# Kernel tuning notes

Hardware: AMD Instinct MI355X
Metric: run time of the kernel (lower is better)

The kernel has to match this reference:

```python
import jax, jax.numpy as jnp
import numpy as np

N = 16384      # total nodes (B graphs x 64 squares)
B = 256        # number of graphs
NODES = 64     # nodes per graph (chess board)
E = 131072     # directed edges (avg degree 8)
F_IN = 128
H = 256
GH = 4         # GAT heads
TH = 8         # transformer heads
L_GNN = 8
L_TF = 6
EPS = 1e-5


def layer_norm(x, g, b):
    m = jnp.mean(x, -1, keepdims=True)
    v = jnp.mean((x - m) ** 2, -1, keepdims=True)
    return (x - m) * jax.lax.rsqrt(v + EPS) * g + b


def setup_inputs() -> dict:
    key = jax.random.key(0)
    ks = iter(jax.random.split(key, 80))

    def nrm(shape, s=0.02):
        return jax.random.normal(next(ks), shape, jnp.float32) * s

    x = jax.random.normal(next(ks), (N, F_IN), jnp.float32)
    gid = jax.random.randint(next(ks), (E,), 0, B)
    off = jax.random.randint(next(ks), (2, E), 0, NODES)
    edge_index = gid[None, :] * NODES + off          # edges stay within a graph
    batch = jnp.arange(N, dtype=jnp.int32) // NODES
    piece_types = jax.random.randint(next(ks), (N,), 1, 7)
    return dict(
        x=x, edge_index=edge_index, batch=batch, piece_types=piece_types,
        emb_w=nrm((H, F_IN)), emb_b=nrm((H,)),
        gat_w=nrm((L_GNN, GH * H, H)), gat_as=nrm((L_GNN, GH, H)),
        gat_ad=nrm((L_GNN, GH, H)), gat_b=nrm((L_GNN, H)),
        gnn_g=jnp.ones((L_GNN, H)), gnn_beta=jnp.zeros((L_GNN, H)),
        ln1_g=jnp.ones((L_TF, H)), ln1_b=jnp.zeros((L_TF, H)),
        in_w=nrm((L_TF, 3 * H, H)), in_b=nrm((L_TF, 3 * H)),
        out_w=nrm((L_TF, H, H)), out_b=nrm((L_TF, H)),
        ln2_g=jnp.ones((L_TF, H)), ln2_b=jnp.zeros((L_TF, H)),
        ff1_w=nrm((L_TF, 4 * H, H)), ff1_b=nrm((L_TF, 4 * H)),
        ff2_w=nrm((L_TF, H, 4 * H)), ff2_b=nrm((L_TF, H)),
        pool_w=nrm((H,)), pool_b=nrm((1,)),
        vw1=nrm((H, H)), vb1=nrm((H,)), vw2=nrm((1, H)), vb2=nrm((1,)),
        pw1=nrm((H, H)), pb1=nrm((H,)), pw2=nrm((H, H)), pb2=nrm((H,)),
        uw1=nrm((H // 2, H)), ub1=nrm((H // 2,)), uw2=nrm((1, H // 2)), ub2=nrm((1,)))


def _forward(x, edge_index, batch, emb_w, emb_b, gat_w, gat_as, gat_ad, gat_b,
             gnn_g, gnn_beta, ln1_g, ln1_b, in_w, in_b, out_w, out_b, ln2_g,
             ln2_b, ff1_w, ff1_b, ff2_w, ff2_b, pool_w, pool_b, vw1, vb1, vw2,
             vb2, pw1, pb1, pw2, pb2, uw1, ub1, uw2, ub2):
    loops = jnp.arange(N, dtype=edge_index.dtype)     # GATConv add_self_loops=True
    src = jnp.concatenate([edge_index[0], loops])
    dst = jnp.concatenate([edge_index[1], loops])
    h = x @ emb_w.T + emb_b                           # [N,H] node embedding

    def gnn_layer(h, p):                              # ResidualGNNLayer
        W, a_s, a_d, bias, g, beta = p
        hp = (h @ W.T).reshape(N, GH, H)              # per-head projection
        al_s = jnp.sum(hp * a_s, -1)                  # [N,GH]
        al_d = jnp.sum(hp * a_d, -1)
        e = jax.nn.leaky_relu(al_s[src] + al_d[dst], 0.2)
        m = jax.ops.segment_max(e, dst, num_segments=N)
        ex = jnp.exp(e - m[dst])                      # segment softmax over dst
        den = jax.ops.segment_sum(ex, dst, num_segments=N)
        alpha = ex / den[dst]
        out = jax.ops.segment_sum(hp[src] * alpha[:, :, None], dst, num_segments=N)
        out = out.mean(1) + bias                      # concat=False -> head mean
        out = jax.nn.gelu(layer_norm(out, g, beta), approximate=False)
        return h + out, None                          # project = Identity

    h, _ = jax.lax.scan(gnn_layer, h, (gat_w, gat_as, gat_ad, gat_b, gnn_g, gnn_beta))

    # nn.MultiheadAttention defaults batch_first=False: axis0 (=B graphs) is the
    # sequence axis, axis1 (=64 nodes) is the batch axis — faithful to the source.
    xt = h.reshape(B, NODES, H)
    HD = H // TH

    def tf_layer(t, p):
        g1, b1, iw, ib, ow, ob, g2, b2, w1, fb1, w2, fb2 = p
        tn = layer_norm(t, g1, b1)
        q, k, v = jnp.split(tn @ iw.T + ib, 3, axis=-1)
        q = q.reshape(B, NODES, TH, HD)
        k = k.reshape(B, NODES, TH, HD)
        v = v.reshape(B, NODES, TH, HD)
        att = jnp.einsum('sbhd,tbhd->bhst', q, k) * (1.0 / HD ** 0.5)
        att = jax.nn.softmax(att, -1)
        o = jnp.einsum('bhst,tbhd->sbhd', att, v).reshape(B, NODES, H)
        t = t + (o @ ow.T + ob)
        tn = layer_norm(t, g2, b2)
        ff = jax.nn.gelu(tn @ w1.T + fb1, approximate=False) @ w2.T + fb2
        return t + ff, None

    xt, _ = jax.lax.scan(tf_layer, xt, (ln1_g, ln1_b, in_w, in_b, out_w, out_b,
                                        ln2_g, ln2_b, ff1_w, ff1_b, ff2_w, ff2_b))
    h = xt.reshape(N, H)

    # global attention pooling: softmax over ALL nodes (dim=0, as in the source)
    aw = jax.nn.softmax(h @ pool_w + pool_b[0], axis=0)
    g_rep = jax.ops.segment_sum(h * aw[:, None], batch, num_segments=B)
    value = jnp.tanh(jax.nn.gelu(g_rep @ vw1.T + vb1, approximate=False) @ vw2.T + vb2)[:, 0]
    policy = jax.nn.gelu(h @ pw1.T + pb1, approximate=False) @ pw2.T + pb2
    unc = jax.nn.softplus(jax.nn.gelu(g_rep @ uw1.T + ub1, approximate=False) @ uw2.T + ub2)[:, 0]
    return value, policy, unc


def reference(x, edge_index, batch, piece_types, emb_w, emb_b, gat_w, gat_as,
              gat_ad, gat_b, gnn_g, gnn_beta, ln1_g, ln1_b, in_w, in_b, out_w,
              out_b, ln2_g, ln2_b, ff1_w, ff1_b, ff2_w, ff2_b, pool_w, pool_b,
              vw1, vb1, vw2, vb2, pw1, pb1, pw2, pb2, uw1, ub1, uw2, ub2):
    # piece_types feeds PositionSpecificFeatureExtractor whose output is dead
    # code in the source forward (never used), so it is omitted here.
    return _forward(x, edge_index, batch, emb_w, emb_b, gat_w, gat_as, gat_ad,
                    gat_b, gnn_g, gnn_beta, ln1_g, ln1_b, in_w, in_b, out_w,
                    out_b, ln2_g, ln2_b, ff1_w, ff1_b, ff2_w, ff2_b, pool_w,
                    pool_b, vw1, vb1, vw2, vb2, pw1, pb1, pw2, pb2, uw1, ub1,
                    uw2, ub2)
```

## Files before the change

### kernel.cpp

```cpp
#include <hip/hip_runtime.h>
#include <hip/hip_bf16.h>

typedef __hip_bfloat16 bf16;
typedef __bf16 bf16x8 __attribute__((ext_vector_type(8)));
typedef float  f32x4  __attribute__((ext_vector_type(4)));

#define N_NODES 16384
#define HDIM    256
#define NE      131072
#define NE2     147456

__device__ __forceinline__ float b2f(bf16 v){ return __bfloat162float(v); }
__device__ __forceinline__ bf16  f2b(float v){ return __float2bfloat16(v); }
__device__ __forceinline__ float us2f(unsigned short u){
  union { unsigned int i; float f; } c; c.i = ((unsigned int)u) << 16; return c.f;
}
__device__ __forceinline__ unsigned short f2us(float f){
  bf16 h = __float2bfloat16(f);
  unsigned short u; __builtin_memcpy(&u, &h, 2); return u;
}
__device__ __forceinline__ float gelu_f(float x){
  return 0.5f * x * (1.0f + erff(x * 0.7071067811865476f));
}
__device__ __forceinline__ float wave_sum(float v){
  #pragma unroll
  for (int o = 32; o > 0; o >>= 1) v += __shfl_xor(v, o);
  return v;
}
__device__ __forceinline__ float wave_max(float v){
  #pragma unroll
  for (int o = 32; o > 0; o >>= 1) v = fmaxf(v, __shfl_xor(v, o));
  return v;
}

__device__ __forceinline__ float4 load4(const float* p){ return *(const float4*)p; }
__device__ __forceinline__ float4 load4(const bf16* p){
  ushort4 u = *(const ushort4*)p;
  return make_float4(us2f(u.x), us2f(u.y), us2f(u.z), us2f(u.w));
}
__device__ __forceinline__ void store4(float* p, float4 v){ *(float4*)p = v; }
__device__ __forceinline__ void store4(bf16* p, float4 v){
  ushort4 u = make_ushort4(f2us(v.x), f2us(v.y), f2us(v.z), f2us(v.w));
  *(ushort4*)p = u;
}
__device__ __forceinline__ void storev(float* p, float4 v){ *(float4*)p = v; }
__device__ __forceinline__ void storev(bf16*  p, float4 v){ store4(p, v); }

__device__ __forceinline__ void async_ld16(const bf16* g, unsigned short* l){
  __builtin_amdgcn_global_load_lds(
      (const __attribute__((address_space(1))) void*)g,
      (__attribute__((address_space(3))) void*)l, 16, 0, 0);
}

__global__ void detect_dtype(const unsigned short* __restrict__ x, int n, int* __restrict__ flags){
  int i = blockIdx.x * 256 + threadIdx.x;
  if (i < n) {
    unsigned short u = x[i];
    if ((u & 0x7F80) == 0x7F80) atomicOr(&flags[1], 1);
  }
}
struct ConvArgs {
  const void* src[35];
  unsigned short* dst[35];
  int cumg[36];
  int n[35];
};
__global__ void conv_all4(ConvArgs a, const int* __restrict__ flags){
  int gi = blockIdx.x * 256 + threadIdx.x;
  if (gi >= a.cumg[35]) return;
  int lo = 0, hi = 34;
  while (lo < hi) { int mid = (lo + hi + 1) >> 1; if (gi >= a.cumg[mid]) lo = mid; else hi = mid - 1; }
  int e0 = (gi - a.cumg[lo]) << 2;
  int n = a.n[lo];
  unsigned short* d = a.dst[lo];
  if (flags[1]) {
    const float* s = (const float*)a.src[lo];
    if (e0 + 4 <= n) {
      float4 v = *(const float4*)(s + e0);
      *(ushort4*)(d + e0) = make_ushort4(f2us(v.x), f2us(v.y), f2us(v.z), f2us(v.w));
    } else {
      for (int t = 0; t < n - e0; ++t) d[e0 + t] = f2us(s[e0 + t]);
    }
  } else {
    const unsigned short* s = (const unsigned short*)a.src[lo];
    if (e0 + 4 <= n) *(ushort4*)(d + e0) = *(const ushort4*)(s + e0);
    else for (int t = 0; t < n - e0; ++t) d[e0 + t] = s[e0 + t];
  }
}
__global__ void emit_out(const unsigned short* __restrict__ stage, void* __restrict__ out,
                         int n, const int* __restrict__ flags){
  int i = blockIdx.x * 256 + threadIdx.x;
  if (i >= n) return;
  if (flags[1]) ((float*)out)[i] = us2f(stage[i]);
  else          ((unsigned short*)out)[i] = stage[i];
}
__global__ void write_sentinel(bf16* out, float v){ out[threadIdx.x] = f2b(v); }

#define GF_GELU 1
#define GF_RES  2
#define GF_MIR  4

template<typename TO, int FLAGS>
__global__ __launch_bounds__(256) void gemm2(
    const bf16* __restrict__ A, const bf16* __restrict__ W,
    const bf16* __restrict__ bias, const float* __restrict__ res,
    TO* __restrict__ C, bf16* __restrict__ C2, int M, int Nn, int K)
{
  __shared__ __align__(16) char ldsraw[36864];
  unsigned short* sA = (unsigned short*)ldsraw;
  unsigned short* sB = sA + 128 * 64;
  const int tid = threadIdx.x;
  const int wave = tid >> 6, lane = tid & 63;
  const int quad = lane >> 4, l16 = lane & 15;
  const int wm = wave & 1, wn = wave >> 1;
  const int row0 = blockIdx.y << 7, col0 = blockIdx.x << 7;
  const int lr = lane >> 3, lc = lane & 7;

  f32x4 acc[4][4] = {};

  for (int kt = 0; kt < K; kt += 64) {
    #pragma unroll
    for (int it = 0; it < 4; ++it) {
      int r0 = (wave << 5) + (it << 3);
      int rr = r0 + lr;
      int gch = lc ^ (rr & 7);
      async_ld16(A + (size_t)(row0 + rr) * K + kt + (gch << 3), sA + (r0 << 6));
      async_ld16(W + (size_t)(col0 + rr) * K + kt + (gch << 3), sB + (r0 << 6));
    }
    __syncthreads();
    #pragma unroll
    for (int kk = 0; kk < 2; ++kk) {
      bf16x8 af[4];
      #pragma unroll
      for (int i = 0; i < 4; ++i) {
        int m = (wm << 6) + (i << 4) + l16;
        af[i] = *(const bf16x8*)&sA[(m << 6) + ((((kk << 2) + quad) ^ (l16 & 7)) << 3)];
      }
      #pragma unroll
      for (int j = 0; j < 4; ++j) {
        int n = (wn << 6) + (j << 4) + l16;
        bf16x8 bfr = *(const bf16x8*)&sB[(n << 6) + ((((kk << 2) + quad) ^ (l16 & 7)) << 3)];
        #pragma unroll
        for (int i = 0; i < 4; ++i)
          acc[i][j] = __builtin_amdgcn_mfma_f32_16x16x32_bf16(af[i], bfr, acc[i][j], 0, 0, 0);
      }
    }
    __syncthreads();
  }

  float* ct = (float*)ldsraw + wave * (64 * 36);
  #pragma unroll
  for (int p = 0; p < 2; ++p) {
    #pragma unroll
    for (int i = 0; i < 4; ++i)
      #pragma unroll
      for (int r = 0; r < 4; ++r) {
        int row = (i << 4) + (quad << 2) + r;
        ct[row * 36 + l16]      = acc[i][(p << 1) + 0][r];
        ct[row * 36 + 16 + l16] = acc[i][(p << 1) + 1][r];
      }
    #pragma unroll
    for (int it2 = 0; it2 < 8; ++it2) {
      int row = (it2 << 3) + lr;
      int c4 = lc << 2;
      float4 v = *(const float4*)&ct[row * 36 + c4];
      int gcol = col0 + (wn << 6) + (p << 5) + c4;
      size_t gidx = (size_t)(row0 + (wm << 6) + row) * Nn + gcol;
      if (bias) {
        float4 bv = load4(bias + gcol);
        v.x += bv.x; v.y += bv.y; v.z += bv.z; v.w += bv.w;
      }
      if (FLAGS & GF_GELU) {
        v.x = gelu_f(v.x); v.y = gelu_f(v.y); v.z = gelu_f(v.z); v.w = gelu_f(v.w);
      }
      if (FLAGS & GF_RES) {
        float4 rv = *(const float4*)&res[gidx];
        v.x += rv.x; v.y += rv.y; v.z += rv.z; v.w += rv.w;
      }
      storev(C + gidx, v);
      if (FLAGS & GF_MIR) store4(C2 + gidx, v);
    }
  }
}

__global__ void csr_count(const int* __restrict__ edst, int* __restrict__ cnt){
  int e = blockIdx.x * 256 + threadIdx.x;
  if (e < NE2) {
    int d = (e < NE) ? edst[e] : (e - NE);
    atomicAdd(&cnt[d], 1);
  }
}
__global__ __launch_bounds__(1024) void csr_scan(const int* __restrict__ cnt, int* __restrict__ off){
  __shared__ int ls[1024];
  int t = threadIdx.x;
  int base = t * 16;
  int loc[16]; int s = 0;
  #pragma unroll
  for (int j = 0; j < 16; ++j) { loc[j] = s; s += cnt[base + j]; }
  ls[t] = s;
  __syncthreads();
  for (int o = 1; o < 1024; o <<= 1) {
    int v = (t >= o) ? ls[t - o] : 0;
    __syncthreads();
    ls[t] += v;
    __syncthreads();
  }
  int pre = (t == 0) ? 0 : ls[t - 1];
  #pragma unroll
  for (int j = 0; j < 16; ++j) off[base + j] = pre + loc[j];
  if (t == 1023) off[N_NODES] = ls[1023];
}
__global__ void csr_fill(const int* __restrict__ edst, const int* __restrict__ off,
                         int* __restrict__ fillc, int* __restrict__ list){
  int e = blockIdx.x * 256 + threadIdx.x;
  if (e < NE2) {
    int d = (e < NE) ? edst[e] : (e - NE);
    int p = atomicAdd(&fillc[d], 1);
    list[off[d] + p] = e;
  }
}

#define ALF_S 68

__device__ __forceinline__ bf16x8 pack8(const float* v, float scale){
  unsigned short u[8];
  #pragma unroll
  for (int t = 0; t < 8; ++t) u[t] = f2us(v[t] * scale);
  bf16x8 r; __builtin_memcpy(&r, u, 16); return r;
}

__global__ __launch_bounds__(256) void gat_graph2(
    const int* __restrict__ esrc, const bf16* __restrict__ hp,
    const int* __restrict__ off, const int* __restrict__ list,
    const bf16* __restrict__ a_s, const bf16* __restrict__ a_d,
    bf16* __restrict__ msg4, int g0, int hn)
{
  __shared__ unsigned short hpT[256 * 64];
  __shared__ float alpha[64 * ALF_S];
  __shared__ float als[64], ald[64], dinv[64];

  const int hd = blockIdx.x & 3;
  const int lg = blockIdx.x >> 2;
  const int g  = g0 + lg;
  const int tid = threadIdx.x;
  const int wave = tid >> 6, lane = tid & 63;
  const int quad = lane >> 4, l16 = lane & 15;
  const int nd = tid >> 2;
  const int k4 = tid & 3;

  {
    const bf16* hrow = hp + ((size_t)((g << 6) + nd)) * 1024 + hd * 256 + (k4 << 6);
    const bf16* asp = a_s + hd * 256 + (k4 << 6);
    const bf16* adp = a_d + hd * 256 + (k4 << 6);
    const int s3 = nd >> 3, s7 = nd & 7;
    float s1 = 0.f, s2 = 0.f;
    #pragma unroll
    for (int jj = 0; jj < 64; jj += 8) {
      ushort4 u0 = *(const ushort4*)(hrow + jj);
      ushort4 u1 = *(const ushort4*)(hrow + jj + 4);
      unsigned short hv[8] = {u0.x, u0.y, u0.z, u0.w, u1.x, u1.y, u1.z, u1.w};
      #pragma unroll
      for (int t = 0; t < 8; ++t) {
        int c = (k4 << 6) + jj + t;
        hpT[(c << 6) + (((s3 ^ (c & 7)) << 3) | s7)] = hv[t];
        float hf = us2f(hv[t]);
        s1 += hf * b2f(asp[jj + t]);
        s2 += hf * b2f(adp[jj + t]);
      }
    }
    s1 += __shfl_xor(s1, 1); s1 += __shfl_xor(s1, 2);
    s2 += __shfl_xor(s2, 1); s2 += __shfl_xor(s2, 2);
    if (k4 == 0) { als[nd] = s1; ald[nd] = s2; }
  }
  #pragma unroll
  for (int idx = tid; idx < 64 * ALF_S; idx += 256) alpha[idx] = 0.f;
  __syncthreads();

  {
    int st = off[(g << 6) + nd];
    int deg = off[(g << 6) + nd + 1] - st;
    float ad = ald[nd];
    float mx = -1e30f;
    for (int e = k4; e < deg; e += 4) {
      int ed = list[st + e];
      int sl = ((ed < NE) ? esrc[ed] : (ed - NE)) - (g << 6);
      float v = als[sl] + ad;
      v = (v > 0.f) ? v : 0.2f * v;
      mx = fmaxf(mx, v);
    }
    mx = fmaxf(mx, __shfl_xor(mx, 1)); mx = fmaxf(mx, __shfl_xor(mx, 2));
    float den = 0.f;
    for (int e = k4; e < deg; e += 4) {
      int ed = list[st + e];
      int sl = ((ed < NE) ? esrc[ed] : (ed - NE)) - (g << 6);
      float v = als[sl] + ad;
      v = (v > 0.f) ? v : 0.2f * v;
      float w = __expf(v - mx);
      den += w;
      atomicAdd(&alpha[nd * ALF_S + sl], w);
    }
    den += __shfl_xor(den, 1); den += __shfl_xor(den, 2);
    if (k4 == 0) dinv[nd] = 1.0f / den;
  }
  __syncthreads();

  f32x4 acc[4][4] = {};
  #pragma unroll
  for (int kk = 0; kk < 2; ++kk) {
    bf16x8 af[4];
    #pragma unroll
    for (int i = 0; i < 4; ++i) {
      int m = (i << 4) + l16;
      const float* ap = &alpha[m * ALF_S + (kk << 5) + (quad << 3)];
      float av[8];
      float4 a0 = *(const float4*)ap, a1 = *(const float4*)(ap + 4);
      av[0]=a0.x; av[1]=a0.y; av[2]=a0.z; av[3]=a0.w;
      av[4]=a1.x; av[5]=a1.y; av[6]=a1.z; av[7]=a1.w;
      af[i] = pack8(av, dinv[m]);
    }
    #pragma unroll
    for (int j = 0; j < 4; ++j) {
      int c2 = (wave << 6) + (j << 4) + l16;
      int chunk = (kk << 2) + quad;
      bf16x8 bfr = *(const bf16x8*)&hpT[(c2 << 6) + ((chunk ^ (c2 & 7)) << 3)];
      #pragma unroll
      for (int i = 0; i < 4; ++i)
        acc[i][j] = __builtin_amdgcn_mfma_f32_16x16x32_bf16(af[i], bfr, acc[i][j], 0, 0, 0);
    }
  }

  #pragma unroll
  for (int j = 0; j < 4; ++j) {
    int col = (wave << 6) + (j << 4) + l16;
    #pragma unroll
    for (int i = 0; i < 4; ++i) {
      int rbase = (i << 4) + (quad << 2);
      #pragma unroll
      for (int r = 0; r < 4; ++r)
        msg4[((size_t)hd * hn + (lg << 6) + rbase + r) * 256 + col] = f2b(acc[i][j][r]);
    }
  }
}

__global__ __launch_bounds__(256) void gat_epi(
    const bf16* __restrict__ msg4, int hn, int n0,
    const bf16* __restrict__ bias, const bf16* __restrict__ gg, const bf16* __restrict__ gb,
    float* __restrict__ h, bf16* __restrict__ hb)
{
  int nl = blockIdx.x * 4 + (threadIdx.x >> 6);
  int lane = threadIdx.x & 63;
  int c = lane * 4;
  float4 s = make_float4(0.f, 0.f, 0.f, 0.f);
  #pragma unroll
  for (int hd = 0; hd < 4; ++hd) {
    float4 m = load4(msg4 + ((size_t)hd * hn + nl) * 256 + c);
    s.x += m.x; s.y += m.y; s.z += m.z; s.w += m.w;
  }
  float4 bv = load4(bias + c);
  float ox = s.x * 0.25f + bv.x, oy = s.y * 0.25f + bv.y;
  float oz = s.z * 0.25f + bv.z, ow = s.w * 0.25f + bv.w;
  float mean = wave_sum(ox + oy + oz + ow) * (1.0f / 256.0f);
  float dx = ox - mean, dy = oy - mean, dz = oz - mean, dw = ow - mean;
  float var = wave_sum(dx*dx + dy*dy + dz*dz + dw*dw) * (1.0f / 256.0f);
  float r = rsqrtf(var + 1e-5f);
  float4 gv = load4(gg + c); float4 b2 = load4(gb + c);
  size_t base = ((size_t)(n0 + nl)) * 256 + c;
  float4 hv = load4(h + base);
  hv.x += gelu_f(dx * r * gv.x + b2.x);
  hv.y += gelu_f(dy * r * gv.y + b2.y);
  hv.z += gelu_f(dz * r * gv.z + b2.z);
  hv.w += gelu_f(dw * r * gv.w + b2.w);
  store4(h + base, hv);
  store4(hb + base, hv);
}

__global__ __launch_bounds__(256) void ln_kernel(
    const float* __restrict__ x, bf16* __restrict__ y,
    const bf16* __restrict__ g, const bf16* __restrict__ b)
{
  int row = blockIdx.x * 4 + (threadIdx.x >> 6);
  int lane = threadIdx.x & 63;
  int c = lane * 4;
  float4 v = load4(x + (size_t)row * 256 + c);
  float mean = wave_sum(v.x + v.y + v.z + v.w) * (1.0f / 256.0f);
  float dx = v.x - mean, dy = v.y - mean, dz = v.z - mean, dw = v.w - mean;
  float var = wave_sum(dx*dx + dy*dy + dz*dz + dw*dw) * (1.0f / 256.0f);
  float r = rsqrtf(var + 1e-5f);
  float4 gv = load4(g + c); float4 bv = load4(b + c);
  store4(y + (size_t)row * 256 + c,
         make_float4(dx*r*gv.x + bv.x, dy*r*gv.y + bv.y, dz*r*gv.z + bv.z, dw*r*gv.w + bv.w));
}

#define VT_LDS 268
#define P_LDS  72

__global__ __launch_bounds__(256) void attn_mfma(
    const bf16* __restrict__ qkv, bf16* __restrict__ obuf)
{
  const int b  = blockIdx.x & 63;
  const int hh = blockIdx.x >> 6;
  __shared__ unsigned short VTs[32 * VT_LDS];
  __shared__ unsigned short Ps[4][64 * P_LDS];
  const int tid  = threadIdx.x;
  const int wave = tid >> 6, lane = tid & 63;
  const int quad = lane >> 4, l16 = lane & 15;

  {
    const bf16* vb = qkv + (size_t)(tid * 64 + b) * 768 + 512 + hh * 32;
    unsigned short vv[32];
    *(uint4*)&vv[0]  = *(const uint4*)(vb);
    *(uint4*)&vv[8]  = *(const uint4*)(vb + 8);
    *(uint4*)&vv[16] = *(const uint4*)(vb + 16);
    *(uint4*)&vv[24] = *(const uint4*)(vb + 24);
    #pragma unroll
    for (int d = 0; d < 32; ++d) VTs[d * VT_LDS + tid] = vv[d];
  }
  bf16x8 qf[4];
  #pragma unroll
  for (int i = 0; i < 4; ++i) {
    int s = (wave << 6) + (i << 4) + l16;
    qf[i] = *(const bf16x8*)(qkv + (size_t)(s * 64 + b) * 768 + hh * 32 + (quad << 3));
  }
  __syncthreads();

  const float scale = 0.17677669529663687f;
  f32x4 oacc[4][2] = {};
  float lsum[4][4] = {};
  unsigned short* Pw = &Ps[wave][0];

  for (int nt = 0; nt < 4; ++nt) {
    bf16x8 kf[4];
    #pragma unroll
    for (int j = 0; j < 4; ++j) {
      int t = (nt << 6) + (j << 4) + l16;
      kf[j] = *(const bf16x8*)(qkv + (size_t)(t * 64 + b) * 768 + 256 + hh * 32 + (quad << 3));
    }
    f32x4 zero = {0.f, 0.f, 0.f, 0.f};
    f32x4 sx[4][4];
    #pragma unroll
    for (int i = 0; i < 4; ++i)
      #pragma unroll
      for (int j = 0; j < 4; ++j)
        sx[i][j] = __builtin_amdgcn_mfma_f32_16x16x32_bf16(qf[i], kf[j], zero, 0, 0, 0);
    #pragma unroll
    for (int i = 0; i < 4; ++i) {
      #pragma unroll
      for (int r = 0; r < 4; ++r) {
        float p[4]; float rs = 0.f;
        #pragma unroll
        for (int j = 0; j < 4; ++j) {
          float sc = fminf(fmaxf(sx[i][j][r] * scale, -60.f), 60.f);
          p[j] = __expf(sc);
          rs += p[j];
        }
        #pragma unroll
        for (int o = 1; o < 16; o <<= 1) rs += __shfl_xor(rs, o);
        lsum[i][r] += rs;
        int row = (i << 4) + (quad << 2) + r;
        #pragma unroll
        for (int j = 0; j < 4; ++j)
          Pw[row * P_LDS + (j << 4) + l16] = f2us(p[j]);
      }
    }
    #pragma unroll
    for (int kk = 0; kk < 2; ++kk) {
      bf16x8 vf[2];
      #pragma unroll
      for (int j2 = 0; j2 < 2; ++j2)
        vf[j2] = *(const bf16x8*)&VTs[((j2 << 4) + l16) * VT_LDS + (nt << 6) + (kk << 5) + (quad << 3)];
      #pragma unroll
      for (int i2 = 0; i2 < 4; ++i2) {
        bf16x8 pf = *(const bf16x8*)&Pw[((i2 << 4) + l16) * P_LDS + (kk << 5) + (quad << 3)];
        #pragma unroll
        for (int j2 = 0; j2 < 2; ++j2)
          oacc[i2][j2] = __builtin_amdgcn_mfma_f32_16x16x32_bf16(pf, vf[j2], oacc[i2][j2], 0, 0, 0);
      }
    }
  }
  #pragma unroll
  for (int i = 0; i < 4; ++i) {
    #pragma unroll
    for (int r = 0; r < 4; ++r) {
      int srow = (wave << 6) + (i << 4) + (quad << 2) + r;
      float inv = 1.0f / lsum[i][r];
      #pragma unroll
      for (int j2 = 0; j2 < 2; ++j2)
        obuf[(size_t)(srow * 64 + b) * 256 + hh * 32 + (j2 << 4) + l16] = f2b(oacc[i][j2][r] * inv);
    }
  }
}

__global__ __launch_bounds__(256) void pool_logit(
    const float* __restrict__ h, const bf16* __restrict__ pw, const bf16* __restrict__ pb,
    float* __restrict__ logits)
{
  int n = blockIdx.x * 4 + (threadIdx.x >> 6); int lane = threadIdx.x & 63;
  float4 hv = load4(h + (size_t)n * 256 + lane * 4);
  float4 wv = load4(pw + lane * 4);
  float acc = wave_sum(hv.x*wv.x + hv.y*wv.y + hv.z*wv.z + hv.w*wv.w);
  if (lane == 0) logits[n] = acc + b2f(pb[0]);
}
__global__ __launch_bounds__(1024) void pool_reduce(
    const float* __restrict__ logits, float* __restrict__ red)
{
  __shared__ float sm[16];
  int t = threadIdx.x;
  float m = -1e30f;
  for (int i = t; i < N_NODES; i += 1024) m = fmaxf(m, logits[i]);
  m = wave_max(m);
  if ((t & 63) == 0) sm[t >> 6] = m;
  __syncthreads();
  if (t == 0) { float mm = sm[0]; for (int i = 1; i < 16; ++i) mm = fmaxf(mm, sm[i]); sm[0] = mm; }
  __syncthreads();
  float gmax = sm[0];
  __syncthreads();
  float s = 0.f;
  for (int i = t; i < N_NODES; i += 1024) s += expf(logits[i] - gmax);
  s = wave_sum(s);
  if ((t & 63) == 0) sm[t >> 6] = s;
  __syncthreads();
  if (t == 0) { float ss = 0.f; for (int i = 0; i < 16; ++i) ss += sm[i]; red[0] = gmax; red[1] = 1.0f / ss; }
}
__global__ __launch_bounds__(256) void pool_grep(
    const float* __restrict__ h, const float* __restrict__ logits,
    const float* __restrict__ red, bf16* __restrict__ g_rep)
{
  __shared__ float w[64];
  int g = blockIdx.x; int tid = threadIdx.x;
  if (tid < 64) w[tid] = expf(logits[g * 64 + tid] - red[0]) * red[1];
  __syncthreads();
  float acc = 0.f;
  for (int nd = 0; nd < 64; ++nd) acc += h[((size_t)g * 64 + nd) * 256 + tid] * w[nd];
  g_rep[(size_t)g * 256 + tid] = f2b(acc);
}
__global__ __launch_bounds__(256) void head_value(
    const float* __restrict__ vt, const bf16* __restrict__ w2, const bf16* __restrict__ b2,
    bf16* __restrict__ out)
{
  int gidx = blockIdx.x * 4 + (threadIdx.x >> 6); int lane = threadIdx.x & 63;
  float acc = 0.f;
  #pragma unroll
  for (int j = 0; j < 4; ++j) { int c = j * 64 + lane; acc += vt[(size_t)gidx * 256 + c] * b2f(w2[c]); }
  acc = wave_sum(acc);
  if (lane == 0) out[gidx] = f2b(tanhf(acc + b2f(b2[0])));
}
__global__ __launch_bounds__(256) void head_unc(
    const float* __restrict__ ut, const bf16* __restrict__ w2, const bf16* __restrict__ b2,
    bf16* __restrict__ out)
{
  int gidx = blockIdx.x * 4 + (threadIdx.x >> 6); int lane = threadIdx.x & 63;
  float acc = 0.f;
  #pragma unroll
  for (int j = 0; j < 2; ++j) { int c = j * 64 + lane; acc += ut[(size_t)gidx * 128 + c] * b2f(w2[c]); }
  acc = wave_sum(acc);
  if (lane == 0) {
    float x = acc + b2f(b2[0]);
    float sp = (x > 20.f) ? x : log1pf(expf(x));
    out[gidx] = f2b(sp);
  }
}

extern "C" void kernel_launch(void* const* d_in, const int* in_sizes, int n_in,
                              void* d_out, int out_size, void* d_ws, size_t ws_size,
                              hipStream_t stream)
{
  (void)out_size;
  const int* eidx = (const int*)d_in[1];

  char* ws = (char*)d_ws;
  size_t wo = 0;
  auto alloc = [&](size_t bytes) -> char* {
    char* p = ws + wo; wo += (bytes + 255) & ~(size_t)255; return p;
  };
  int*   flags = (int*)alloc(256);
  int*   cnt   = (int*)alloc((size_t)N_NODES * 4);
  int*   fillc = (int*)alloc((size_t)N_NODES * 4);
  size_t zero_end = wo;

  bf16* conv[38] = {};
  static const int fidx[35] = {0,4,5,6,7,8,9,10,11,12,13,14,15,16,17,18,19,
                               20,21,22,23,24,25,26,27,28,29,30,31,32,33,34,35,36,37};
  for (int j = 0; j < 35; ++j) {
    int idx = fidx[j];
    conv[idx] = (bf16*)alloc((size_t)in_sizes[idx] * 2);
  }
  float* h     = (float*)alloc((size_t)N_NODES * 256 * 4);
  bf16*  hb    = (bf16*) alloc((size_t)N_NODES * 256 * 2);
  bf16*  big   = (bf16*) alloc((size_t)N_NODES * 1024 * 2);
  const int OUT_ELEMS = 256 + N_NODES * 256 + 256;
  bf16*  tn     = (bf16*)alloc((size_t)N_NODES * 256 * 2);
  bf16*  ostage = (bf16*)alloc((size_t)OUT_ELEMS * 2);
  int*   off   = (int*)alloc((size_t)(N_NODES + 1) * 4);
  int*   list  = (int*)alloc((size_t)NE2 * 4);
  float* logits= (float*)alloc((size_t)N_NODES * 4);
  float* redb  = (float*)alloc(256);
  bf16*  g_rep = (bf16*)alloc((size_t)256 * 256 * 2);
  float* val_t = (float*)alloc((size_t)256 * 256 * 4);
  float* unc_t = (float*)alloc((size_t)256 * 128 * 4);
  size_t base_needed = wo;

  if (n_in != 38)                   { write_sentinel<<<1,256,0,stream>>>((bf16*)d_out, 4.f);  return; }
  if (in_sizes[0] != N_NODES * 128) { write_sentinel<<<1,256,0,stream>>>((bf16*)d_out, 8.f);  return; }
  if (in_sizes[1] != 2 * NE)        { write_sentinel<<<1,256,0,stream>>>((bf16*)d_out, 16.f); return; }
  if (ws_size < base_needed)        { write_sentinel<<<1,256,0,stream>>>((bf16*)d_out, 32.f); return; }

  size_t msg_bytes = (size_t)4 * N_NODES * 256 * 2;
  bf16* msg4; int halves;
  if (ws_size >= base_needed + msg_bytes + 256) {
    msg4 = (bf16*)alloc(msg_bytes); halves = 1;
  } else {
    msg4 = tn; halves = 2;
  }

  hipMemsetAsync(d_ws, 0, zero_end, stream);

  detect_dtype<<<256, 256, 0, stream>>>((const unsigned short*)d_in[0], 65536, flags);
  {
    ConvArgs ca;
    int cum = 0;
    for (int j = 0; j < 35; ++j) {
      int idx = fidx[j];
      ca.src[j] = d_in[idx];
      ca.dst[j] = (unsigned short*)conv[idx];
      ca.cumg[j] = cum;
      ca.n[j] = in_sizes[idx];
      cum += (in_sizes[idx] + 3) >> 2;
    }
    ca.cumg[35] = cum;
    conv_all4<<<(cum + 255) / 256, 256, 0, stream>>>(ca, flags);
  }
  const bf16 *xb = conv[0], *emb_w = conv[4], *emb_b = conv[5], *gat_w = conv[6],
             *gat_as = conv[7], *gat_ad = conv[8], *gat_b = conv[9], *gnn_g = conv[10],
             *gnn_beta = conv[11], *ln1_g = conv[12], *ln1_b = conv[13], *in_w = conv[14],
             *in_b = conv[15], *out_w = conv[16], *out_b = conv[17], *ln2_g = conv[18],
             *ln2_b = conv[19], *ff1_w = conv[20], *ff1_b = conv[21], *ff2_w = conv[22],
             *ff2_b = conv[23], *pool_w = conv[24], *pool_b = conv[25],
             *vw1 = conv[26], *vb1 = conv[27], *vw2 = conv[28], *vb2 = conv[29],
             *pw1 = conv[30], *pb1 = conv[31], *pw2 = conv[32], *pb2 = conv[33],
             *uw1 = conv[34], *ub1 = conv[35], *uw2 = conv[36], *ub2 = conv[37];

  bf16* qkv  = big;
  bf16* obuf = big + (size_t)N_NODES * 768;
  bf16* hp   = big;
  bf16* ffb  = big;
  bf16* o_val = ostage;
  bf16* o_pol = ostage + 256;
  bf16* o_unc = ostage + 256 + (size_t)N_NODES * 256;

  csr_count<<<(NE2 + 255) / 256, 256, 0, stream>>>(eidx + NE, cnt);
  csr_scan<<<1, 1024, 0, stream>>>(cnt, off);
  csr_fill<<<(NE2 + 255) / 256, 256, 0, stream>>>(eidx + NE, off, fillc, list);

  gemm2<float, GF_MIR><<<dim3(2, 128), 256, 0, stream>>>(
      xb, emb_w, emb_b, nullptr, h, hb, N_NODES, 256, 128);

  const int gph = 256 / halves;
  const int hn  = N_NODES / halves;
  for (int l = 0; l < 8; ++l) {
    gemm2<bf16, 0><<<dim3(8, 128), 256, 0, stream>>>(
        hb, gat_w + (size_t)l * 1024 * 256, nullptr, nullptr, hp, nullptr, N_NODES, 1024, 256);
    for (int ph = 0; ph < halves; ++ph) {
      gat_graph2<<<gph * 4, 256, 0, stream>>>(eidx, hp, off, list,
          gat_as + l * 1024, gat_ad + l * 1024, msg4, ph * gph, hn);
      gat_epi<<<hn / 4, 256, 0, stream>>>(msg4, hn, ph * hn,
          gat_b + l * 256, gnn_g + l * 256, gnn_beta + l * 256, h, hb);
    }
  }

  for (int l = 0; l < 6; ++l) {
    ln_kernel<<<N_NODES / 4, 256, 0, stream>>>(h, tn, ln1_g + l * 256, ln1_b + l * 256);
    gemm2<bf16, 0><<<dim3(6, 128), 256, 0, stream>>>(
        tn, in_w + (size_t)l * 768 * 256, in_b + l * 768, nullptr, qkv, nullptr, N_NODES, 768, 256);
    attn_mfma<<<512, 256, 0, stream>>>(qkv, obuf);
    gemm2<float, GF_RES><<<dim3(2, 128), 256, 0, stream>>>(
        obuf, out_w + (size_t)l * 256 * 256, out_b + l * 256, h, h, nullptr, N_NODES, 256, 256);
    ln_kernel<<<N_NODES / 4, 256, 0, stream>>>(h, tn, ln2_g + l * 256, ln2_b + l * 256);
    gemm2<bf16, GF_GELU><<<dim3(8, 128), 256, 0, stream>>>(
        tn, ff1_w + (size_t)l * 1024 * 256, ff1_b + l * 1024, nullptr, ffb, nullptr, N_NODES, 1024, 256);
    if (l < 5)
      gemm2<float, GF_RES><<<dim3(2, 128), 256, 0, stream>>>(
          ffb, ff2_w + (size_t)l * 256 * 1024, ff2_b + l * 256, h, h, nullptr, N_NODES, 256, 1024);
    else
      gemm2<float, GF_RES | GF_MIR><<<dim3(2, 128), 256, 0, stream>>>(
          ffb, ff2_w + (size_t)l * 256 * 1024, ff2_b + l * 256, h, h, hb, N_NODES, 256, 1024);
  }

  pool_logit<<<N_NODES / 4, 256, 0, stream>>>(h, pool_w, pool_b, logits);
  pool_reduce<<<1, 1024, 0, stream>>>(logits, redb);
  pool_grep<<<256, 256, 0, stream>>>(h, logits, redb, g_rep);
  gemm2<float, GF_GELU><<<dim3(2, 2), 256, 0, stream>>>(
      g_rep, vw1, vb1, nullptr, val_t, nullptr, 256, 256, 256);
  head_value<<<64, 256, 0, stream>>>(val_t, vw2, vb2, o_val);
  gemm2<float, GF_GELU><<<dim3(1, 2), 256, 0, stream>>>(
      g_rep, uw1, ub1, nullptr, unc_t, nullptr, 256, 128, 256);
  head_unc<<<64, 256, 0, stream>>>(unc_t, uw2, ub2, o_unc);
  gemm2<bf16, GF_GELU><<<dim3(2, 128), 256, 0, stream>>>(
      hb, pw1, pb1, nullptr, tn, nullptr, N_NODES, 256, 256);
  gemm2<bf16, 0><<<dim3(2, 128), 256, 0, stream>>>(
      tn, pw2, pb2, nullptr, o_pol, nullptr, N_NODES, 256, 256);

  emit_out<<<(OUT_ELEMS + 255) / 256, 256, 0, stream>>>(
      (const unsigned short*)ostage, d_out, OUT_ELEMS, flags);
}
```

Measured before the change: 1.621 ms.

## Compute GAT projection transposed and fuse attention-score dot products into GEMM epilogue

The GAT projection GEMM now swaps operands to produce a feature-major (transposed) hp layout, so gat_graph2 can load its transposed tile with async 16-byte copies instead of scattering per-element stores into LDS. The per-node source/destination attention dot products are computed in the GEMM epilogue as partial sums over row slices, written to a side buffer, and summed in gat_graph2. This removes the per-element dot-product and transpose work from the graph kernel. In exchange it adds shuffle reductions and extra global partial-sum traffic to the GEMM, and the dot products now use fp32 pre-rounding values rather than bf16-rounded hp.

```diff
diff --git a/kernel.cpp b/kernel.cpp
--- a/kernel.cpp
+++ b/kernel.cpp
@@ -99,12 +99,15 @@
 #define GF_GELU 1
 #define GF_RES  2
 #define GF_MIR  4
+#define GF_ALS  8
 
 template<typename TO, int FLAGS>
 __global__ __launch_bounds__(256) void gemm2(
     const bf16* __restrict__ A, const bf16* __restrict__ W,
     const bf16* __restrict__ bias, const float* __restrict__ res,
-    TO* __restrict__ C, bf16* __restrict__ C2, int M, int Nn, int K)
+    TO* __restrict__ C, bf16* __restrict__ C2, int M, int Nn, int K,
+    const bf16* __restrict__ asp, const bf16* __restrict__ adp,
+    float* __restrict__ alsp)
 {
   __shared__ __align__(16) char ldsraw[36864];
   unsigned short* sA = (unsigned short*)ldsraw;
@@ -159,6 +162,8 @@
         ct[row * 36 + l16]      = acc[i][(p << 1) + 0][r];
         ct[row * 36 + 16 + l16] = acc[i][(p << 1) + 1][r];
       }
+    float4 sS = make_float4(0.f, 0.f, 0.f, 0.f);
+    float4 sD = make_float4(0.f, 0.f, 0.f, 0.f);
     #pragma unroll
     for (int it2 = 0; it2 < 8; ++it2) {
       int row = (it2 << 3) + lr;
@@ -166,6 +171,12 @@
       float4 v = *(const float4*)&ct[row * 36 + c4];
       int gcol = col0 + (wn << 6) + (p << 5) + c4;
       size_t gidx = (size_t)(row0 + (wm << 6) + row) * Nn + gcol;
+      if (FLAGS & GF_ALS) {
+        float asv = b2f(asp[row0 + (wm << 6) + row]);
+        float adv = b2f(adp[row0 + (wm << 6) + row]);
+        sS.x += asv * v.x; sS.y += asv * v.y; sS.z += asv * v.z; sS.w += asv * v.w;
+        sD.x += adv * v.x; sD.y += adv * v.y; sD.z += adv * v.z; sD.w += adv * v.w;
+      }
       if (bias) {
         float4 bv = load4(bias + gcol);
         v.x += bv.x; v.y += bv.y; v.z += bv.z; v.w += bv.w;
@@ -179,6 +190,22 @@
       }
       storev(C + gidx, v);
       if (FLAGS & GF_MIR) store4(C2 + gidx, v);
+    }
+    if (FLAGS & GF_ALS) {
+      #pragma unroll
+      for (int o = 8; o < 64; o <<= 1) {
+        sS.x += __shfl_xor(sS.x, o); sS.y += __shfl_xor(sS.y, o);
+        sS.z += __shfl_xor(sS.z, o); sS.w += __shfl_xor(sS.w, o);
+        sD.x += __shfl_xor(sD.x, o); sD.y += __shfl_xor(sD.y, o);
+        sD.z += __shfl_xor(sD.z, o); sD.w += __shfl_xor(sD.w, o);
+      }
+      if (lr == 0) {
+        int node = col0 + (wn << 6) + (p << 5) + (lc << 2);
+        int hd2 = blockIdx.y >> 1;
+        int slice = ((blockIdx.y & 1) << 1) | wm;
+        *(float4*)&alsp[(size_t)((slice << 3) + hd2) * Nn + node] = sS;
+        *(float4*)&alsp[(size_t)((slice << 3) + 4 + hd2) * Nn + node] = sD;
+      }
     }
   }
 }
@@ -230,9 +257,9 @@
 }
 
 __global__ __launch_bounds__(256) void gat_graph2(
-    const int* __restrict__ esrc, const bf16* __restrict__ hp,
+    const int* __restrict__ esrc, const bf16* __restrict__ hpT_g,
     const int* __restrict__ off, const int* __restrict__ list,
-    const bf16* __restrict__ a_s, const bf16* __restrict__ a_d,
+    const float* __restrict__ alsp,
     bf16* __restrict__ msg4, int g0, int hn)
 {
   __shared__ unsigned short hpT[256 * 64];
@@ -249,28 +276,22 @@
   const int k4 = tid & 3;
 
   {
-    const bf16* hrow = hp + ((size_t)((g << 6) + nd)) * 1024 + hd * 256 + (k4 << 6);
-    const bf16* asp = a_s + hd * 256 + (k4 << 6);
-    const bf16* adp = a_d + hd * 256 + (k4 << 6);
-    const int s3 = nd >> 3, s7 = nd & 7;
-    float s1 = 0.f, s2 = 0.f;
-    #pragma unroll
-    for (int jj = 0; jj < 64; jj += 8) {
-      ushort4 u0 = *(const ushort4*)(hrow + jj);
-      ushort4 u1 = *(const ushort4*)(hrow + jj + 4);
-      unsigned short hv[8] = {u0.x, u0.y, u0.z, u0.w, u1.x, u1.y, u1.z, u1.w};
-      #pragma unroll
-      for (int t = 0; t < 8; ++t) {
-        int c = (k4 << 6) + jj + t;
-        hpT[(c << 6) + (((s3 ^ (c & 7)) << 3) | s7)] = hv[t];
-        float hf = us2f(hv[t]);
-        s1 += hf * b2f(asp[jj + t]);
-        s2 += hf * b2f(adp[jj + t]);
-      }
-    }
-    s1 += __shfl_xor(s1, 1); s1 += __shfl_xor(s1, 2);
-    s2 += __shfl_xor(s2, 1); s2 += __shfl_xor(s2, 2);
-    if (k4 == 0) { als[nd] = s1; ald[nd] = s2; }
+    const int rl = lane >> 3, jj = lane & 7;
+    #pragma unroll
+    for (int it = 0; it < 8; ++it) {
+      int c = (it << 5) + (wave << 3) + rl;
+      async_ld16(hpT_g + (size_t)((hd << 8) + c) * 16384 + (g << 6) + ((jj ^ (c & 7)) << 3),
+                 hpT + (((it << 5) + (wave << 3)) << 6));
+    }
+  }
+  if (tid < 128) {
+    int n2 = tid & 63;
+    int sd = (tid >> 6) << 2;
+    float v = 0.f;
+    #pragma unroll
+    for (int sl = 0; sl < 4; ++sl)
+      v += alsp[(size_t)((sl << 3) + sd + hd) * 16384 + (g << 6) + n2];
+    if (sd) ald[n2] = v; else als[n2] = v;
   }
   #pragma unroll
   for (int idx = tid; idx < 64 * ALF_S; idx += 256) alpha[idx] = 0.f;
@@ -597,6 +618,7 @@
   bf16*  g_rep = (bf16*)alloc((size_t)256 * 256 * 2);
   float* val_t = (float*)alloc((size_t)256 * 256 * 4);
   float* unc_t = (float*)alloc((size_t)256 * 128 * 4);
+  float* alsp  = (float*)alloc((size_t)32 * N_NODES * 4);
   size_t base_needed = wo;
 
   if (n_in != 38)                   { write_sentinel<<<1,256,0,stream>>>((bf16*)d_out, 4.f);  return; }
@@ -641,7 +663,7 @@
 
   bf16* qkv  = big;
   bf16* obuf = big + (size_t)N_NODES * 768;
-  bf16* hp   = big;
+  bf16* hpT_g = big;
   bf16* ffb  = big;
   bf16* o_val = ostage;
   bf16* o_pol = ostage + 256;
@@ -652,16 +674,18 @@
   csr_fill<<<(NE2 + 255) / 256, 256, 0, stream>>>(eidx + NE, off, fillc, list);
 
   gemm2<float, GF_MIR><<<dim3(2, 128), 256, 0, stream>>>(
-      xb, emb_w, emb_b, nullptr, h, hb, N_NODES, 256, 128);
+      xb, emb_w, emb_b, nullptr, h, hb, N_NODES, 256, 128,
+      nullptr, nullptr, nullptr);
 
   const int gph = 256 / halves;
   const int hn  = N_NODES / halves;
   for (int l = 0; l < 8; ++l) {
-    gemm2<bf16, 0><<<dim3(8, 128), 256, 0, stream>>>(
-        hb, gat_w + (size_t)l * 1024 * 256, nullptr, nullptr, hp, nullptr, N_NODES, 1024, 256);
+    gemm2<bf16, GF_ALS><<<dim3(128, 8), 256, 0, stream>>>(
+        gat_w + (size_t)l * 1024 * 256, hb, nullptr, nullptr, hpT_g, nullptr,
+        1024, N_NODES, 256, gat_as + l * 1024, gat_ad + l * 1024, alsp);
     for (int ph = 0; ph < halves; ++ph) {
-      gat_graph2<<<gph * 4, 256, 0, stream>>>(eidx, hp, off, list,
-          gat_as + l * 1024, gat_ad + l * 1024, msg4, ph * gph, hn);
+      gat_graph2<<<gph * 4, 256, 0, stream>>>(eidx, hpT_g, off, list, alsp,
+          msg4, ph * gph, hn);
       gat_epi<<<hn / 4, 256, 0, stream>>>(msg4, hn, ph * hn,
           gat_b + l * 256, gnn_g + l * 256, gnn_beta + l * 256, h, hb);
     }
@@ -670,34 +694,43 @@
   for (int l = 0; l < 6; ++l) {
     ln_kernel<<<N_NODES / 4, 256, 0, stream>>>(h, tn, ln1_g + l * 256, ln1_b + l * 256);
     gemm2<bf16, 0><<<dim3(6, 128), 256, 0, stream>>>(
-        tn, in_w + (size_t)l * 768 * 256, in_b + l * 768, nullptr, qkv, nullptr, N_NODES, 768, 256);
+        tn, in_w + (size_t)l * 768 * 256, in_b + l * 768, nullptr, qkv, nullptr, N_NODES, 768, 256,
+        nullptr, nullptr, nullptr);
     attn_mfma<<<512, 256, 0, stream>>>(qkv, obuf);
     gemm2<float, GF_RES><<<dim3(2, 128), 256, 0, stream>>>(
-        obuf, out_w + (size_t)l * 256 * 256, out_b + l * 256, h, h, nullptr, N_NODES, 256, 256);
+        obuf, out_w + (size_t)l * 256 * 256, out_b + l * 256, h, h, nullptr, N_NODES, 256, 256,
+        nullptr, nullptr, nullptr);
     ln_kernel<<<N_NODES / 4, 256, 0, stream>>>(h, tn, ln2_g + l * 256, ln2_b + l * 256);
     gemm2<bf16, GF_GELU><<<dim3(8, 128), 256, 0, stream>>>(
-        tn, ff1_w + (size_t)l * 1024 * 256, ff1_b + l * 1024, nullptr, ffb, nullptr, N_NODES, 1024, 256);
+        tn, ff1_w + (size_t)l * 1024 * 256, ff1_b + l * 1024, nullptr, ffb, nullptr, N_NODES, 1024, 256,
+        nullptr, nullptr, nullptr);
     if (l < 5)
       gemm2<float, GF_RES><<<dim3(2, 128), 256, 0, stream>>>(
-          ffb, ff2_w + (size_t)l * 256 * 1024, ff2_b + l * 256, h, h, nullptr, N_NODES, 256, 1024);
+          ffb, ff2_w + (size_t)l * 256 * 1024, ff2_b + l * 256, h, h, nullptr, N_NODES, 256, 1024,
+          nullptr, nullptr, nullptr);
     else
       gemm2<float, GF_RES | GF_MIR><<<dim3(2, 128), 256, 0, stream>>>(
-          ffb, ff2_w + (size_t)l * 256 * 1024, ff2_b + l * 256, h, h, hb, N_NODES, 256, 1024);
+          ffb, ff2_w + (size_t)l * 256 * 1024, ff2_b + l * 256, h, h, hb, N_NODES, 256, 1024,
+          nullptr, nullptr, nullptr);
   }
 
   pool_logit<<<N_NODES / 4, 256, 0, stream>>>(h, pool_w, pool_b, logits);
   pool_reduce<<<1, 1024, 0, stream>>>(logits, redb);
   pool_grep<<<256, 256, 0, stream>>>(h, logits, redb, g_rep);
   gemm2<float, GF_GELU><<<dim3(2, 2), 256, 0, stream>>>(
-      g_rep, vw1, vb1, nullptr, val_t, nullptr, 256, 256, 256);
+      g_rep, vw1, vb1, nullptr, val_t, nullptr, 256, 256, 256,
+      nullptr, nullptr, nullptr);
   head_value<<<64, 256, 0, stream>>>(val_t, vw2, vb2, o_val);
   gemm2<float, GF_GELU><<<dim3(1, 2), 256, 0, stream>>>(
-      g_rep, uw1, ub1, nullptr, unc_t, nullptr, 256, 128, 256);
+      g_rep, uw1, ub1, nullptr, unc_t, nullptr, 256, 128, 256,
+      nullptr, nullptr, nullptr);
   head_unc<<<64, 256, 0, stream>>>(unc_t, uw2, ub2, o_unc);
   gemm2<bf16, GF_GELU><<<dim3(2, 128), 256, 0, stream>>>(
-      hb, pw1, pb1, nullptr, tn, nullptr, N_NODES, 256, 256);
+      hb, pw1, pb1, nullptr, tn, nullptr, N_NODES, 256, 256,
+      nullptr, nullptr, nullptr);
   gemm2<bf16, 0><<<dim3(2, 128), 256, 0, stream>>>(
-      tn, pw2, pb2, nullptr, o_pol, nullptr, N_NODES, 256, 256);
+      tn, pw2, pb2, nullptr, o_pol, nullptr, N_NODES, 256, 256,
+      nullptr, nullptr, nullptr);
 
   emit_out<<<(OUT_ELEMS + 255) / 256, 256, 0, stream>>>(
       (const unsigned short*)ostage, d_out, OUT_ELEMS, flags);
```

Result: faster. 1.582 ms (-2.4%).
